# Performance work log

Hardware: AMD Instinct MI355X
Metric: run time of the kernel (lower is better)

The kernel has to match this reference:

```python
import jax, jax.numpy as jnp
import numpy as np

N_HEADS = 16
HEAD_DIM = 64  # dim=1024 / n_heads=16


def setup_inputs() -> dict:
    key = jax.random.key(0)
    ks = jax.random.split(key, 7)
    B, S, D = 4, 2048, 1024
    scale = 1.0 / np.sqrt(D)
    return {
        "q": jax.random.normal(ks[0], (B, S, D), jnp.float32),
        "k": jax.random.normal(ks[1], (B, S, D), jnp.float32),
        "v": jax.random.normal(ks[2], (B, S, D), jnp.float32),
        "Wq": jax.random.normal(ks[3], (D, D), jnp.float32) * scale,
        "Wk": jax.random.normal(ks[4], (D, D), jnp.float32) * scale,
        "Wv": jax.random.normal(ks[5], (D, D), jnp.float32) * scale,
        "Wo": jax.random.normal(ks[6], (D, D), jnp.float32) * scale,
    }


def reference(q, k, v, Wq, Wk, Wv, Wo):
    B, S, _ = q.shape
    H, Dh = N_HEADS, HEAD_DIM
    # linear projections (torch Linear: x @ W.T), reshape to [B, H, S, Dh]
    xq = (q @ Wq.T).reshape(B, S, H, Dh).transpose(0, 2, 1, 3)
    xk = (k @ Wk.T).reshape(B, S, H, Dh).transpose(0, 2, 1, 3)
    xv = (v @ Wv.T).reshape(B, S, H, Dh).transpose(0, 2, 1, 3)
    scores = jnp.einsum("bhsd,bhtd->bhst", xq, xk) / jnp.sqrt(jnp.float32(Dh))
    # causal mask: -inf above diagonal
    causal = jnp.triu(jnp.full((S, S), -jnp.inf, jnp.float32), k=1)
    scores = scores + causal[None, None]
    attn = jax.nn.softmax(scores.astype(jnp.float32), axis=-1).astype(xq.dtype)
    out = jnp.einsum("bhst,bhtd->bhsd", attn, xv)
    out = out.transpose(0, 2, 1, 3).reshape(B, S, H * Dh)
    return out @ Wo.T
```

## Files before the change

kernel.cpp:

```cpp
#include <hip/hip_runtime.h>
#include <hip/hip_bf16.h>

#define DI __device__ __forceinline__

typedef __attribute__((ext_vector_type(8))) short short8;
typedef __attribute__((ext_vector_type(4))) short short4v;
typedef __attribute__((ext_vector_type(4))) float f32x4;

#define QSCALE 0.180336885f

DI short f2bf(float f) {
  __hip_bfloat16 h = __float2bfloat16(f);
  return __builtin_bit_cast(short, h);
}

DI float fexp2(float x) {
#if __has_builtin(__builtin_amdgcn_exp2f)
  return __builtin_amdgcn_exp2f(x);
#else
  return exp2f(x);
#endif
}

DI void gl16(const short* g, short* l) {
  __builtin_amdgcn_global_load_lds(
      (const __attribute__((address_space(1))) void*)g,
      (__attribute__((address_space(3))) void*)l, 16, 0, 0);
}

__global__ __launch_bounds__(256) void convert_all(
    const float* __restrict__ q, const float* __restrict__ k,
    const float* __restrict__ v, const float* __restrict__ wq,
    const float* __restrict__ wk, const float* __restrict__ wv,
    const float* __restrict__ wo, short* __restrict__ qb,
    short* __restrict__ kb, short* __restrict__ vb, short* __restrict__ wb) {
  int z = blockIdx.z;
  const float* src;
  short* dst;
  if (z < 3) {
    src = (z == 0) ? q : (z == 1) ? k : v;
    dst = (z == 0) ? qb : (z == 1) ? kb : vb;
  } else {
    if (blockIdx.x >= 512) return;
    src = (z == 3) ? wq : (z == 4) ? wk : (z == 5) ? wv : wo;
    dst = wb + (size_t)(z - 3) * 1024 * 1024;
  }
  size_t i = ((size_t)blockIdx.x * 256 + threadIdx.x) * 8;
  float4 f0 = *(const float4*)(src + i);
  float4 f1 = *(const float4*)(src + i + 4);
  short8 o;
  o[0] = f2bf(f0.x); o[1] = f2bf(f0.y); o[2] = f2bf(f0.z); o[3] = f2bf(f0.w);
  o[4] = f2bf(f1.x); o[5] = f2bf(f1.y); o[6] = f2bf(f1.z); o[7] = f2bf(f1.w);
  *(short8*)(dst + i) = o;
}

__global__ __launch_bounds__(256) void convert_one(
    const float* __restrict__ src, short* __restrict__ dst) {
  size_t i = ((size_t)blockIdx.x * 256 + threadIdx.x) * 8;
  float4 f0 = *(const float4*)(src + i);
  float4 f1 = *(const float4*)(src + i + 4);
  short8 o;
  o[0] = f2bf(f0.x); o[1] = f2bf(f0.y); o[2] = f2bf(f0.z); o[3] = f2bf(f0.w);
  o[4] = f2bf(f1.x); o[5] = f2bf(f1.y); o[6] = f2bf(f1.z); o[7] = f2bf(f1.w);
  *(short8*)(dst + i) = o;
}

enum { OUT_F32 = 0, OUT_HEAD = 1, OUT_HEADT = 2 };

DI void stage_half(const short* __restrict__ g, short* lds, int bmn, int k0,
                   int half, int wid_, int lrr, int lch) {
  int r0 = half * 128 + wid_ * 8;
#pragma unroll
  for (int i = 0; i < 2; ++i) {
    int rb = r0 + i * 64;
    int rr = rb + lrr;
    int sc = (lch ^ (rr & 7)) << 3;
    gl16(g + (size_t)(bmn + rr) * 1024 + k0 + sc, lds + rb * 64);
  }
}

template <int OMODE, int Q>
DI void do_quad(const char* bufA, const short8 (&bfr)[4][2],
                f32x4 (&acc)[8][4], int wm, int l15, int lq) {
  short8 afr[2][2];
#pragma unroll
  for (int i = 0; i < 2; ++i)
#pragma unroll
    for (int ks = 0; ks < 2; ++ks) {
      int row = wm * 128 + (Q * 2 + i) * 16 + l15;
      int off = (row * 128 + ks * 64 + lq * 16) ^ ((row & 7) << 4);
      afr[i][ks] = *(const short8*)(bufA + off);
    }
  __builtin_amdgcn_s_setprio(1);
#pragma unroll
  for (int i = 0; i < 2; ++i)
#pragma unroll
    for (int nt = 0; nt < 4; ++nt)
#pragma unroll
      for (int ks = 0; ks < 2; ++ks) {
        if (OMODE == OUT_HEADT)
          acc[Q * 2 + i][nt] = __builtin_amdgcn_mfma_f32_16x16x32_bf16(
              bfr[nt][ks], afr[i][ks], acc[Q * 2 + i][nt], 0, 0, 0);
        else
          acc[Q * 2 + i][nt] = __builtin_amdgcn_mfma_f32_16x16x32_bf16(
              afr[i][ks], bfr[nt][ks], acc[Q * 2 + i][nt], 0, 0, 0);
      }
  __builtin_amdgcn_s_setprio(0);
}

template <int OMODE>
DI void gemm256_core(short* sA, short* sB, const short* __restrict__ A,
                     const short* __restrict__ B, void* __restrict__ Cp,
                     float scale, int bm, int bn) {
  const int tid = threadIdx.x;
  const int lane = tid & 63;
  const int wid = tid >> 6;
  const int wm = wid >> 2, wn = wid & 3;
  const int l15 = lane & 15, lq = lane >> 4;
  const int lrr = lane >> 3, lch = lane & 7;

  f32x4 acc[8][4] = {};

  stage_half(A, sA, bm, 0, 0, wid, lrr, lch);
  stage_half(A, sA, bm, 0, 1, wid, lrr, lch);
  stage_half(B, sB, bn, 0, 0, wid, lrr, lch);
  stage_half(B, sB, bn, 0, 1, wid, lrr, lch);
  stage_half(A, sA + 16384, bm, 64, 0, wid, lrr, lch);
  stage_half(A, sA + 16384, bm, 64, 1, wid, lrr, lch);
  stage_half(B, sB + 16384, bn, 64, 0, wid, lrr, lch);
  stage_half(B, sB + 16384, bn, 64, 1, wid, lrr, lch);
  asm volatile("s_waitcnt vmcnt(8)" ::: "memory");
  __builtin_amdgcn_s_barrier();

  for (int k = 0; k < 16; ++k) {
    const char* bufA = (const char*)(sA + (k & 1) * 16384);
    const char* bufB = (const char*)(sB + (k & 1) * 16384);
    short* stA = sA + ((k + 1) & 1) * 16384;
    short* stB = sB + (k & 1) * 16384;
    const bool stgA = (k >= 1 && k < 15);
    const bool stgB = (k < 14);

    short8 bfr[4][2];
    if (stgA) stage_half(A, stA, bm, (k + 1) * 64, 0, wid, lrr, lch);
#pragma unroll
    for (int nt = 0; nt < 4; ++nt)
#pragma unroll
      for (int ks = 0; ks < 2; ++ks) {
        int row = wn * 64 + nt * 16 + l15;
        int off = (row * 128 + ks * 64 + lq * 16) ^ ((row & 7) << 4);
        bfr[nt][ks] = *(const short8*)(bufB + off);
      }
    do_quad<OMODE, 0>(bufA, bfr, acc, wm, l15, lq);
    __builtin_amdgcn_s_barrier();
    if (stgA) stage_half(A, stA, bm, (k + 1) * 64, 1, wid, lrr, lch);
    if (stgB) stage_half(B, stB, bn, (k + 2) * 64, 0, wid, lrr, lch);
    do_quad<OMODE, 1>(bufA, bfr, acc, wm, l15, lq);
    __builtin_amdgcn_s_barrier();
    if (stgB) stage_half(B, stB, bn, (k + 2) * 64, 1, wid, lrr, lch);
    do_quad<OMODE, 2>(bufA, bfr, acc, wm, l15, lq);
    __builtin_amdgcn_s_barrier();
    do_quad<OMODE, 3>(bufA, bfr, acc, wm, l15, lq);
    if (k < 14) {
      asm volatile("s_waitcnt vmcnt(4)" ::: "memory");
      __builtin_amdgcn_s_barrier();
    } else if (k == 14) {
      asm volatile("s_waitcnt vmcnt(0)" ::: "memory");
      __builtin_amdgcn_s_barrier();
    }
  }

#pragma unroll
  for (int mt = 0; mt < 8; ++mt)
#pragma unroll
    for (int nt = 0; nt < 4; ++nt)
#pragma unroll
      for (int r = 0; r < 4; ++r) {
        float val = acc[mt][nt][r] * scale;
        if (OMODE == OUT_HEADT) {
          int f = bn + wn * 64 + nt * 16 + lq * 4 + r;
          int t = bm + wm * 128 + mt * 16 + l15;
          int bb = t >> 11, s = t & 2047;
          int h = f >> 6, dh = f & 63;
          ((short*)Cp)[((size_t)((bb * 16 + h) * 64 + dh)) * 2048 + s] = f2bf(val);
        } else {
          int rowg = bm + wm * 128 + mt * 16 + lq * 4 + r;
          int colg = bn + wn * 64 + nt * 16 + l15;
          int bb = rowg >> 11, s = rowg & 2047;
          int h = colg >> 6, dh = colg & 63;
          ((short*)Cp)[((size_t)(bb * 16 + h) * 2048 + s) * 64 + dh] = f2bf(val);
        }
      }
}

__global__ __launch_bounds__(512, 1) void proj_gemm256(
    const short* __restrict__ qb, const short* __restrict__ kb,
    const short* __restrict__ vb, const short* __restrict__ wq,
    const short* __restrict__ wk, const short* __restrict__ wv,
    short* __restrict__ xq, short* __restrict__ xk, short* __restrict__ xvT) {
  __shared__ __align__(16) short sA[2 * 256 * 64];
  __shared__ __align__(16) short sB[2 * 256 * 64];
  int gid = blockIdx.x;
  int xcd = gid & 7, slot = gid >> 3;
  int pg = xcd + 8 * (slot >> 2);
  int ntile = slot & 3;
  int z = pg >> 5, pm = pg & 31;
  int bm = pm * 256, bn = ntile * 256;
  if (z == 0)
    gemm256_core<OUT_HEAD>(sA, sB, qb, wq, xq, QSCALE, bm, bn);
  else if (z == 1)
    gemm256_core<OUT_HEAD>(sA, sB, kb, wk, xk, 1.0f, bm, bn);
  else
    gemm256_core<OUT_HEADT>(sA, sB, vb, wv, xvT, 1.0f, bm, bn);
}

DI void stage_tile(const short* __restrict__ A, const short* __restrict__ B,
                   short* dA, short* dB, int bm, int bn, int k0, int wid,
                   int lrr, int lch) {
#pragma unroll
  for (int i = 0; i < 4; ++i) {
    int r0 = wid * 32 + i * 8;
    int rr = r0 + lrr;
    int sc = (lch ^ (rr & 7)) << 3;
    gl16(A + (size_t)(bm + rr) * 1024 + k0 + sc, dA + r0 * 64);
    gl16(B + (size_t)(bn + rr) * 1024 + k0 + sc, dB + r0 * 64);
  }
}

template <int OMODE>
DI void gemm_core(short* sA, short* sB, const short* __restrict__ A,
                  const short* __restrict__ B, void* __restrict__ Cp,
                  float scale, int bm, int bn) {
  const int tid = threadIdx.x;
  const int lane = tid & 63;
  const int wid = tid >> 6;
  const int wm = wid >> 1, wn = wid & 1;
  const int l15 = lane & 15, lq = lane >> 4;
  const int lrr = lane >> 3;
  const int lch = lane & 7;

  f32x4 acc[4][4] = {};

  stage_tile(A, B, sA, sB, bm, bn, 0, wid, lrr, lch);

  int cur = 0;
  for (int t = 0; t < 16; ++t) {
    if (t < 15) {
      stage_tile(A, B, sA + (cur ^ 1) * 8192, sB + (cur ^ 1) * 8192, bm, bn,
                 (t + 1) * 64, wid, lrr, lch);
      asm volatile("s_waitcnt vmcnt(8)" ::: "memory");
    } else {
      asm volatile("s_waitcnt vmcnt(0)" ::: "memory");
    }
    __builtin_amdgcn_s_barrier();

    const char* bA = (const char*)(sA + cur * 8192);
    const char* bB = (const char*)(sB + cur * 8192);
#pragma unroll
    for (int ks = 0; ks < 2; ++ks) {
      short8 a[4], b[4];
#pragma unroll
      for (int mt = 0; mt < 4; ++mt) {
        int row = wm * 64 + mt * 16 + l15;
        int off = (row * 128 + ks * 64 + lq * 16) ^ ((row & 7) << 4);
        a[mt] = *(const short8*)(bA + off);
      }
#pragma unroll
      for (int nt = 0; nt < 4; ++nt) {
        int row = wn * 64 + nt * 16 + l15;
        int off = (row * 128 + ks * 64 + lq * 16) ^ ((row & 7) << 4);
        b[nt] = *(const short8*)(bB + off);
      }
#pragma unroll
      for (int mt = 0; mt < 4; ++mt)
#pragma unroll
        for (int nt = 0; nt < 4; ++nt) {
          if (OMODE == OUT_HEADT)
            acc[mt][nt] = __builtin_amdgcn_mfma_f32_16x16x32_bf16(
                b[nt], a[mt], acc[mt][nt], 0, 0, 0);
          else
            acc[mt][nt] = __builtin_amdgcn_mfma_f32_16x16x32_bf16(
                a[mt], b[nt], acc[mt][nt], 0, 0, 0);
        }
    }
    __builtin_amdgcn_s_barrier();
    cur ^= 1;
  }

#pragma unroll
  for (int mt = 0; mt < 4; ++mt) {
#pragma unroll
    for (int nt = 0; nt < 4; ++nt) {
#pragma unroll
      for (int r = 0; r < 4; ++r) {
        float val = acc[mt][nt][r] * scale;
        if (OMODE == OUT_HEADT) {
          int f = bn + wn * 64 + nt * 16 + lq * 4 + r;
          int t = bm + wm * 64 + mt * 16 + l15;
          int bb = t >> 11, s = t & 2047;
          int h = f >> 6, dh = f & 63;
          ((short*)Cp)[((size_t)((bb * 16 + h) * 64 + dh)) * 2048 + s] = f2bf(val);
        } else {
          int rowg = bm + wm * 64 + mt * 16 + lq * 4 + r;
          int colg = bn + wn * 64 + nt * 16 + l15;
          if (OMODE == OUT_HEAD) {
            int bb = rowg >> 11, s = rowg & 2047;
            int h = colg >> 6, dh = colg & 63;
            ((short*)Cp)[((size_t)(bb * 16 + h) * 2048 + s) * 64 + dh] = f2bf(val);
          } else {
            ((float*)Cp)[(size_t)rowg * 1024 + colg] = val;
          }
        }
      }
    }
  }
}

DI void xcd_map(int id, int& bm, int& bn) {
  int xcd = id & 7, slot = id >> 3;
  int panel = xcd + 8 * (slot >> 3);
  int ntile = slot & 7;
  bm = panel * 128;
  bn = ntile * 128;
}

#define GEMM_LDS()                                  \
  __shared__ __align__(16) short sA[2 * 128 * 64];  \
  __shared__ __align__(16) short sB[2 * 128 * 64];

__global__ __launch_bounds__(256) void proj_oneN(
    const short* __restrict__ A, const short* __restrict__ B,
    short* __restrict__ C, float scale) {
  GEMM_LDS();
  int bm, bn;
  xcd_map(blockIdx.x, bm, bn);
  gemm_core<OUT_HEAD>(sA, sB, A, B, C, scale, bm, bn);
}

__global__ __launch_bounds__(256) void proj_oneT(
    const short* __restrict__ A, const short* __restrict__ B,
    short* __restrict__ C, float scale) {
  GEMM_LDS();
  int bm, bn;
  xcd_map(blockIdx.x, bm, bn);
  gemm_core<OUT_HEADT>(sA, sB, A, B, C, scale, bm, bn);
}

__global__ __launch_bounds__(256) void final_gemm(
    const short* __restrict__ oa, const short* __restrict__ wo,
    float* __restrict__ out) {
  GEMM_LDS();
  int bm, bn;
  xcd_map(blockIdx.x, bm, bn);
  gemm_core<OUT_F32>(sA, sB, oa, wo, out, 1.0f, bm, bn);
}

__global__ __launch_bounds__(512, 4) void attn_k(
    const short* __restrict__ Xq, const short* __restrict__ Xk,
    const short* __restrict__ XvT, short* __restrict__ Oa) {
  __shared__ __align__(16) short sK[2][64 * 64];
  __shared__ __align__(16) short sVT[2][64 * 64];
  __shared__ __align__(16) short sP[8][16 * 64];

  const int tid = threadIdx.x;
  const int lane = tid & 63;
  const int wid = tid >> 6;
  const int l15 = lane & 15, lq = lane >> 4;
  const int bid = blockIdx.x;
  const int ipair = bid >> 6;
  const int bh = bid & 63;
  const int b = bh >> 4, h = bh & 15;

  const short* Q = Xq + (size_t)bh * 2048 * 64;
  const short* K = Xk + (size_t)bh * 2048 * 64;
  const short* VT = XvT + (size_t)bh * 64 * 2048;

  const int srow = tid >> 3;
  const int scol = (tid & 7) * 8;
  const int soff = (srow * 128 + scol * 2) ^ ((srow & 7) << 4);

  short8 kreg, vreg;
  kreg = *(const short8*)(K + (size_t)srow * 64 + scol);
  vreg = *(const short8*)(VT + (size_t)srow * 2048 + scol);

  *(short8*)((char*)sK[0] + soff) = kreg;
  *(short8*)((char*)sVT[0] + soff) = vreg;

  short* sPw = sP[wid];
  int p = 0;

  for (int seg = 0; seg < 2; ++seg) {
    const int qt = seg ? ipair : (15 - ipair);
    const int qfirst = qt * 128 + wid * 16;
    const int qg = qfirst + l15;
    const int qlast = qfirst + 15;
    const int ntile = 2 * qt + 2;

    short8 qf[2];
#pragma unroll
    for (int ks = 0; ks < 2; ++ks)
      qf[ks] = *(const short8*)(Q + (size_t)qg * 64 + ks * 32 + lq * 8);

    float m_run = -1e30f, l_run = 0.f;
    f32x4 acc[4] = {};

    for (int kt = 0; kt < ntile; ++kt) {
      const int kv0 = kt * 64;
      __syncthreads();

      int nkt = kt + 1, nseg = seg;
      if (nkt >= ntile) { nseg = seg + 1; nkt = 0; }
      const bool hn = (nseg < 2);
      if (hn) {
        const int kn = nkt * 64;
        kreg = *(const short8*)(K + (size_t)(kn + srow) * 64 + scol);
        vreg = *(const short8*)(VT + (size_t)srow * 2048 + kn + scol);
      }

      const bool fullmask = (kv0 > qlast);
      if (!fullmask) {
        const bool needmask = (kv0 + 63 > qfirst);
        const char* bufK = (const char*)sK[p];
        const char* bufV = (const char*)sVT[p];

        f32x4 sc[4] = {};
        __builtin_amdgcn_s_setprio(1);
#pragma unroll
        for (int ks = 0; ks < 2; ++ks) {
          short8 kf[4];
#pragma unroll
          for (int nt = 0; nt < 4; ++nt) {
            int row = nt * 16 + l15;
            int off = (row * 128 + ks * 64 + lq * 16) ^ ((row & 7) << 4);
            kf[nt] = *(const short8*)(bufK + off);
          }
#pragma unroll
          for (int nt = 0; nt < 4; ++nt)
            sc[nt] = __builtin_amdgcn_mfma_f32_16x16x32_bf16(kf[nt], qf[ks],
                                                             sc[nt], 0, 0, 0);
        }
        __builtin_amdgcn_s_setprio(0);

        float pv[4][4];
        float m = -1e30f;
        if (needmask) {
#pragma unroll
          for (int nt = 0; nt < 4; ++nt)
#pragma unroll
            for (int r = 0; r < 4; ++r) {
              float s = sc[nt][r];
              if (kv0 + nt * 16 + lq * 4 + r > qg) s = -1e30f;
              pv[nt][r] = s;
              m = fmaxf(m, s);
            }
        } else {
#pragma unroll
          for (int nt = 0; nt < 4; ++nt)
#pragma unroll
            for (int r = 0; r < 4; ++r) {
              float s = sc[nt][r];
              pv[nt][r] = s;
              m = fmaxf(m, s);
            }
        }
        m = fmaxf(m, __shfl_xor(m, 16));
        m = fmaxf(m, __shfl_xor(m, 32));

        if (!__all(m - m_run <= 8.0f)) {
          const float m_new = fmaxf(m_run, m);
          const float corr = fexp2(m_run - m_new);
          l_run *= corr;
#pragma unroll
          for (int mt = 0; mt < 4; ++mt)
#pragma unroll
            for (int r = 0; r < 4; ++r) acc[mt][r] *= corr;
          m_run = m_new;
        }

        float rsum = 0.f;
#pragma unroll
        for (int nt = 0; nt < 4; ++nt)
#pragma unroll
          for (int r = 0; r < 4; ++r) {
            float e = fexp2(pv[nt][r] - m_run);
            pv[nt][r] = e;
            rsum += e;
          }
        rsum += __shfl_xor(rsum, 16);
        rsum += __shfl_xor(rsum, 32);
        l_run += rsum;

#pragma unroll
        for (int nt = 0; nt < 4; ++nt) {
          short4v pw;
#pragma unroll
          for (int r = 0; r < 4; ++r) pw[r] = f2bf(pv[nt][r]);
          int off = (l15 * 128 + nt * 32 + lq * 8) ^ ((l15 & 7) << 4);
          *(short4v*)((char*)sPw + off) = pw;
        }

        __builtin_amdgcn_s_setprio(1);
#pragma unroll
        for (int ks = 0; ks < 2; ++ks) {
          int poff = (l15 * 128 + ks * 64 + lq * 16) ^ ((l15 & 7) << 4);
          short8 pf = *(const short8*)((const char*)sPw + poff);
#pragma unroll
          for (int mt = 0; mt < 4; ++mt) {
            int row = mt * 16 + l15;
            int voff = (row * 128 + ks * 64 + lq * 16) ^ ((row & 7) << 4);
            short8 vf = *(const short8*)(bufV + voff);
            acc[mt] = __builtin_amdgcn_mfma_f32_16x16x32_bf16(vf, pf, acc[mt],
                                                              0, 0, 0);
          }
        }
        __builtin_amdgcn_s_setprio(0);
      }

      if (hn) {
        *(short8*)((char*)sK[p ^ 1] + soff) = kreg;
        *(short8*)((char*)sVT[p ^ 1] + soff) = vreg;
      }
      p ^= 1;
    }

    const float rl = 1.0f / l_run;
    short* orow = Oa + ((size_t)(b * 2048 + qg)) * 1024 + h * 64;
#pragma unroll
    for (int mt = 0; mt < 4; ++mt) {
      short4v o;
#pragma unroll
      for (int r = 0; r < 4; ++r) o[r] = f2bf(acc[mt][r] * rl);
      *(short4v*)(orow + mt * 16 + lq * 4) = o;
    }
  }
}

extern "C" void kernel_launch(void* const* d_in, const int* in_sizes, int n_in,
                              void* d_out, int out_size, void* d_ws,
                              size_t ws_size, hipStream_t stream) {
  const float* q = (const float*)d_in[0];
  const float* k = (const float*)d_in[1];
  const float* v = (const float*)d_in[2];
  const float* Wq = (const float*)d_in[3];
  const float* Wk = (const float*)d_in[4];
  const float* Wv = (const float*)d_in[5];
  const float* Wo = (const float*)d_in[6];

  char* ws = (char*)d_ws;
  short* wq_b = (short*)(ws + (0ull << 20));
  short* wk_b = (short*)(ws + (2ull << 20));
  short* wv_b = (short*)(ws + (4ull << 20));
  short* wo_b = (short*)(ws + (6ull << 20));
  short* xq  = (short*)(ws + (8ull << 20));
  short* xk  = (short*)(ws + (24ull << 20));
  short* xvT = (short*)(ws + (56ull << 20));

  if (ws_size >= (122ull << 20)) {
    short* qb = (short*)(ws + (72ull << 20));
    short* kb = (short*)(ws + (88ull << 20));
    short* vb = (short*)(ws + (104ull << 20));
    short* oa = qb;

    convert_all<<<dim3(4096, 1, 7), 256, 0, stream>>>(q, k, v, Wq, Wk, Wv, Wo,
                                                      qb, kb, vb, wq_b);
    proj_gemm256<<<dim3(384), 512, 0, stream>>>(qb, kb, vb, wq_b, wk_b, wv_b,
                                                xq, xk, xvT);
    attn_k<<<dim3(512), 512, 0, stream>>>(xq, xk, xvT, oa);
    final_gemm<<<dim3(512), 256, 0, stream>>>(oa, wo_b, (float*)d_out);
  } else {
    short* X = (short*)(ws + (8ull << 20));
    short* xq2 = (short*)(ws + (24ull << 20));
    short* xk2 = (short*)(ws + (40ull << 20));
    short* xvT2 = (short*)(ws + (56ull << 20));
    short* oa2 = (short*)(ws + (72ull << 20));

    convert_one<<<dim3(512), 256, 0, stream>>>(Wq, wq_b);
    convert_one<<<dim3(512), 256, 0, stream>>>(Wk, wk_b);
    convert_one<<<dim3(512), 256, 0, stream>>>(Wv, wv_b);
    convert_one<<<dim3(512), 256, 0, stream>>>(Wo, wo_b);
    convert_one<<<dim3(4096), 256, 0, stream>>>(q, X);
    proj_oneN<<<dim3(512), 256, 0, stream>>>(X, wq_b, xq2, QSCALE);
    convert_one<<<dim3(4096), 256, 0, stream>>>(k, X);
    proj_oneN<<<dim3(512), 256, 0, stream>>>(X, wk_b, xk2, 1.0f);
    convert_one<<<dim3(4096), 256, 0, stream>>>(v, X);
    proj_oneT<<<dim3(512), 256, 0, stream>>>(X, wv_b, xvT2, 1.0f);
    attn_k<<<dim3(512), 512, 0, stream>>>(xq2, xk2, xvT2, oa2);
    final_gemm<<<dim3(512), 256, 0, stream>>>(oa2, wo_b, (float*)d_out);
  }
}
```

Baseline: 191.7 us.

## Restructure 256x256 projection GEMM into 8-wave ping-pong band schedule

Rewrites the projection GEMM main loop. Each wave now covers two 64-row bands, with a per-band split of the A fragments and a two-half split of the B fragments, instead of a 128-row strip processed in four quads. Global-to-LDS staging now prefetches only one k-tile ahead for both A and B, interleaved across four phases separated by barriers. The aim is to overlap LDS fragment loads with MFMA clusters, reduce register pressure from fragment buffers, and use a simpler pipeline. The shallower prefetch and the added barriers may expose more global-memory latency.

```diff
diff --git a/kernel.cpp b/kernel.cpp
--- a/kernel.cpp
+++ b/kernel.cpp
@@ -79,31 +79,46 @@
   }
 }
 
-template <int OMODE, int Q>
-DI void do_quad(const char* bufA, const short8 (&bfr)[4][2],
-                f32x4 (&acc)[8][4], int wm, int l15, int lq) {
-  short8 afr[2][2];
-#pragma unroll
-  for (int i = 0; i < 2; ++i)
+DI void loadA_band(const char* bA, short8 (&afr)[4][2], int band, int wm,
+                   int l15, int lq) {
+#pragma unroll
+  for (int mt = 0; mt < 4; ++mt)
 #pragma unroll
     for (int ks = 0; ks < 2; ++ks) {
-      int row = wm * 128 + (Q * 2 + i) * 16 + l15;
+      int row = band * 128 + wm * 64 + mt * 16 + l15;
       int off = (row * 128 + ks * 64 + lq * 16) ^ ((row & 7) << 4);
-      afr[i][ks] = *(const short8*)(bufA + off);
-    }
+      afr[mt][ks] = *(const short8*)(bA + off);
+    }
+}
+
+DI void loadB_band(const char* bB, short8 (&bfr)[2][2], int nb, int wn,
+                   int l15, int lq) {
+#pragma unroll
+  for (int nt = 0; nt < 2; ++nt)
+#pragma unroll
+    for (int ks = 0; ks < 2; ++ks) {
+      int row = wn * 64 + nb * 32 + nt * 16 + l15;
+      int off = (row * 128 + ks * 64 + lq * 16) ^ ((row & 7) << 4);
+      bfr[nt][ks] = *(const short8*)(bB + off);
+    }
+}
+
+template <int OMODE, int BAND, int NB>
+DI void mfma16(f32x4 (&acc)[2][4][4], const short8 (&afr)[4][2],
+               const short8 (&bfr)[2][2]) {
   __builtin_amdgcn_s_setprio(1);
 #pragma unroll
-  for (int i = 0; i < 2; ++i)
-#pragma unroll
-    for (int nt = 0; nt < 4; ++nt)
+  for (int mt = 0; mt < 4; ++mt)
+#pragma unroll
+    for (int nt = 0; nt < 2; ++nt)
 #pragma unroll
       for (int ks = 0; ks < 2; ++ks) {
         if (OMODE == OUT_HEADT)
-          acc[Q * 2 + i][nt] = __builtin_amdgcn_mfma_f32_16x16x32_bf16(
-              bfr[nt][ks], afr[i][ks], acc[Q * 2 + i][nt], 0, 0, 0);
+          acc[BAND][mt][NB * 2 + nt] = __builtin_amdgcn_mfma_f32_16x16x32_bf16(
+              bfr[nt][ks], afr[mt][ks], acc[BAND][mt][NB * 2 + nt], 0, 0, 0);
         else
-          acc[Q * 2 + i][nt] = __builtin_amdgcn_mfma_f32_16x16x32_bf16(
-              afr[i][ks], bfr[nt][ks], acc[Q * 2 + i][nt], 0, 0, 0);
+          acc[BAND][mt][NB * 2 + nt] = __builtin_amdgcn_mfma_f32_16x16x32_bf16(
+              afr[mt][ks], bfr[nt][ks], acc[BAND][mt][NB * 2 + nt], 0, 0, 0);
       }
   __builtin_amdgcn_s_setprio(0);
 }
@@ -119,77 +134,82 @@
   const int l15 = lane & 15, lq = lane >> 4;
   const int lrr = lane >> 3, lch = lane & 7;
 
-  f32x4 acc[8][4] = {};
-
+  f32x4 acc[2][4][4] = {};
+  short8 afr[4][2], bfr[2][2];
+
+  stage_half(B, sB, bn, 0, 0, wid, lrr, lch);
+  stage_half(B, sB, bn, 0, 1, wid, lrr, lch);
   stage_half(A, sA, bm, 0, 0, wid, lrr, lch);
   stage_half(A, sA, bm, 0, 1, wid, lrr, lch);
-  stage_half(B, sB, bn, 0, 0, wid, lrr, lch);
-  stage_half(B, sB, bn, 0, 1, wid, lrr, lch);
-  stage_half(A, sA + 16384, bm, 64, 0, wid, lrr, lch);
-  stage_half(A, sA + 16384, bm, 64, 1, wid, lrr, lch);
-  stage_half(B, sB + 16384, bn, 64, 0, wid, lrr, lch);
-  stage_half(B, sB + 16384, bn, 64, 1, wid, lrr, lch);
-  asm volatile("s_waitcnt vmcnt(8)" ::: "memory");
+  asm volatile("s_waitcnt vmcnt(2)" ::: "memory");
   __builtin_amdgcn_s_barrier();
 
   for (int k = 0; k < 16; ++k) {
-    const char* bufA = (const char*)(sA + (k & 1) * 16384);
-    const char* bufB = (const char*)(sB + (k & 1) * 16384);
-    short* stA = sA + ((k + 1) & 1) * 16384;
-    short* stB = sB + (k & 1) * 16384;
-    const bool stgA = (k >= 1 && k < 15);
-    const bool stgB = (k < 14);
-
-    short8 bfr[4][2];
-    if (stgA) stage_half(A, stA, bm, (k + 1) * 64, 0, wid, lrr, lch);
-#pragma unroll
-    for (int nt = 0; nt < 4; ++nt)
-#pragma unroll
-      for (int ks = 0; ks < 2; ++ks) {
-        int row = wn * 64 + nt * 16 + l15;
-        int off = (row * 128 + ks * 64 + lq * 16) ^ ((row & 7) << 4);
-        bfr[nt][ks] = *(const short8*)(bufB + off);
-      }
-    do_quad<OMODE, 0>(bufA, bfr, acc, wm, l15, lq);
-    __builtin_amdgcn_s_barrier();
-    if (stgA) stage_half(A, stA, bm, (k + 1) * 64, 1, wid, lrr, lch);
-    if (stgB) stage_half(B, stB, bn, (k + 2) * 64, 0, wid, lrr, lch);
-    do_quad<OMODE, 1>(bufA, bfr, acc, wm, l15, lq);
-    __builtin_amdgcn_s_barrier();
-    if (stgB) stage_half(B, stB, bn, (k + 2) * 64, 1, wid, lrr, lch);
-    do_quad<OMODE, 2>(bufA, bfr, acc, wm, l15, lq);
-    __builtin_amdgcn_s_barrier();
-    do_quad<OMODE, 3>(bufA, bfr, acc, wm, l15, lq);
-    if (k < 14) {
+    const char* bA = (const char*)(sA + (k & 1) * 16384);
+    const char* bB = (const char*)(sB + (k & 1) * 16384);
+    short* tA = sA + ((k + 1) & 1) * 16384;
+    short* tB = sB + ((k + 1) & 1) * 16384;
+    const bool stg = (k < 15);
+    const int k1 = (k + 1) * 64;
+
+    if (stg) stage_half(B, tB, bn, k1, 0, wid, lrr, lch);
+    loadA_band(bA, afr, 0, wm, l15, lq);
+    loadB_band(bB, bfr, 0, wn, l15, lq);
+    __builtin_amdgcn_s_barrier();
+    mfma16<OMODE, 0, 0>(acc, afr, bfr);
+    __builtin_amdgcn_s_barrier();
+
+    if (stg) stage_half(B, tB, bn, k1, 1, wid, lrr, lch);
+    loadB_band(bB, bfr, 1, wn, l15, lq);
+    __builtin_amdgcn_s_barrier();
+    mfma16<OMODE, 0, 1>(acc, afr, bfr);
+    if (stg)
       asm volatile("s_waitcnt vmcnt(4)" ::: "memory");
+    else
+      asm volatile("s_waitcnt vmcnt(0)" ::: "memory");
+    __builtin_amdgcn_s_barrier();
+
+    if (stg) stage_half(A, tA, bm, k1, 0, wid, lrr, lch);
+    loadA_band(bA, afr, 1, wm, l15, lq);
+    __builtin_amdgcn_s_barrier();
+    mfma16<OMODE, 1, 1>(acc, afr, bfr);
+    __builtin_amdgcn_s_barrier();
+
+    if (stg) stage_half(A, tA, bm, k1, 1, wid, lrr, lch);
+    loadB_band(bB, bfr, 0, wn, l15, lq);
+    __builtin_amdgcn_s_barrier();
+    mfma16<OMODE, 1, 0>(acc, afr, bfr);
+    if (k < 15) {
+      asm volatile("s_waitcnt vmcnt(2)" ::: "memory");
       __builtin_amdgcn_s_barrier();
-    } else if (k == 14) {
-      asm volatile("s_waitcnt vmcnt(0)" ::: "memory");
-      __builtin_amdgcn_s_barrier();
-    }
-  }
-
-#pragma unroll
-  for (int mt = 0; mt < 8; ++mt)
-#pragma unroll
-    for (int nt = 0; nt < 4; ++nt)
-#pragma unroll
-      for (int r = 0; r < 4; ++r) {
-        float val = acc[mt][nt][r] * scale;
-        if (OMODE == OUT_HEADT) {
-          int f = bn + wn * 64 + nt * 16 + lq * 4 + r;
-          int t = bm + wm * 128 + mt * 16 + l15;
-          int bb = t >> 11, s = t & 2047;
-          int h = f >> 6, dh = f & 63;
-          ((short*)Cp)[((size_t)((bb * 16 + h) * 64 + dh)) * 2048 + s] = f2bf(val);
-        } else {
-          int rowg = bm + wm * 128 + mt * 16 + lq * 4 + r;
-          int colg = bn + wn * 64 + nt * 16 + l15;
-          int bb = rowg >> 11, s = rowg & 2047;
-          int h = colg >> 6, dh = colg & 63;
-          ((short*)Cp)[((size_t)(bb * 16 + h) * 2048 + s) * 64 + dh] = f2bf(val);
-        }
-      }
+    }
+  }
+
+#pragma unroll
+  for (int band = 0; band < 2; ++band)
+#pragma unroll
+    for (int mt = 0; mt < 4; ++mt)
+#pragma unroll
+      for (int j = 0; j < 4; ++j)
+#pragma unroll
+        for (int r = 0; r < 4; ++r) {
+          float val = acc[band][mt][j][r] * scale;
+          if (OMODE == OUT_HEADT) {
+            int f = bn + wn * 64 + j * 16 + lq * 4 + r;
+            int t = bm + band * 128 + wm * 64 + mt * 16 + l15;
+            int bb = t >> 11, s = t & 2047;
+            int h = f >> 6, dh = f & 63;
+            ((short*)Cp)[((size_t)((bb * 16 + h) * 64 + dh)) * 2048 + s] =
+                f2bf(val);
+          } else {
+            int rowg = bm + band * 128 + wm * 64 + mt * 16 + lq * 4 + r;
+            int colg = bn + wn * 64 + j * 16 + l15;
+            int bb = rowg >> 11, s = rowg & 2047;
+            int h = colg >> 6, dh = colg & 63;
+            ((short*)Cp)[((size_t)(bb * 16 + h) * 2048 + s) * 64 + dh] =
+                f2bf(val);
+          }
+        }
 }
 
 __global__ __launch_bounds__(512, 1) void proj_gemm256(
```

After: 199.5 us. 4.1% more time.
